# Kernel optimization log

Measured on AMD Instinct MI355X. Metric: run time of the kernel, lower is better.

Reference implementation:

```python
import jax, jax.numpy as jnp
import numpy as np

HEADS = 8
DIM_HEAD = 64
DOWN = 2

def setup_inputs() -> dict:
    key = jax.random.key(0)
    ks = jax.random.split(key, 6)
    shp = (1, 128, 16, 32, 32)
    inner = HEADS * DIM_HEAD  # 512
    return {
        "x": jax.random.normal(ks[0], shp, dtype=jnp.float32),
        "context": jax.random.normal(ks[1], shp, dtype=jnp.float32),
        "Wq": jax.random.normal(ks[2], (inner, 128), dtype=jnp.float32) * 0.02,
        "Wk": jax.random.normal(ks[3], (inner, 128), dtype=jnp.float32) * 0.02,
        "Wv": jax.random.normal(ks[4], (inner, 128), dtype=jnp.float32) * 0.02,
        "Wo": jax.random.normal(ks[5], (128, inner), dtype=jnp.float32) * 0.02,
    }

def _avg_pool3d(c, f):
    b, ch, d, h, w = c.shape
    return c.reshape(b, ch, d // f, f, h // f, f, w // f, f).mean(axis=(3, 5, 7))

def reference(x, context, Wq, Wk, Wv, Wo):
    b, c, d1, h1, w1 = x.shape
    n = d1 * h1 * w1
    scale = DIM_HEAD ** -0.5
    xf = x.reshape(b, c, n)  # [b, c, N]
    # 1x1x1 conv == channel matmul
    q = jnp.einsum('oc,bcn->bon', Wq, xf).reshape(b, HEADS, DIM_HEAD, n)
    q = jnp.swapaxes(q, -2, -1)  # [b, h, N, dh]
    ctx = _avg_pool3d(context, DOWN)
    _, _, d2, h2, w2 = ctx.shape
    m = d2 * h2 * w2
    cf = ctx.reshape(b, c, m)
    k = jnp.einsum('oc,bcm->bom', Wk, cf).reshape(b, HEADS, DIM_HEAD, m)  # [b,h,dh,M]
    v = jnp.einsum('oc,bcm->bom', Wv, cf).reshape(b, HEADS, DIM_HEAD, m)
    v = jnp.swapaxes(v, -2, -1)  # [b, h, M, dh]
    scores = jnp.einsum('bhnd,bhdm->bhnm', q, k) * scale  # [b,h,N,M]
    attn = jax.nn.softmax(scores, axis=-1)
    out = jnp.einsum('bhnm,bhmd->bhnd', attn, v)  # [b,h,N,dh]
    out = jnp.swapaxes(out, -2, -1).reshape(b, HEADS * DIM_HEAD, n)  # [b,inner,N]
    y = jnp.einsum('oc,bcn->bon', Wo, out)
    return y.reshape(b, -1, d1, h1, w1)
```

## Files before the change

kernel.cpp:

```cpp
#include <hip/hip_runtime.h>

#define N_TOK 16384
#define M_TOK 2048
#define NHEADS 8
#define DH 64
#define CIN 128
#define INNER 512

typedef __attribute__((ext_vector_type(8))) short bf16x8;
typedef __attribute__((ext_vector_type(16))) float f32x16;
typedef __attribute__((ext_vector_type(4))) unsigned int u32x4;
typedef __attribute__((ext_vector_type(2))) unsigned int u32x2;

__device__ __forceinline__ unsigned short f2bf(float f) {
    unsigned u = __float_as_uint(f);
    u += 0x7fff + ((u >> 16) & 1);
    return (unsigned short)(u >> 16);
}

__device__ __forceinline__ unsigned cvtpk(float lo, float hi) {
    unsigned r;
    asm("v_cvt_pk_bf16_f32 %0, %1, %2" : "=v"(r) : "v"(lo), "v"(hi));
    return r;
}

__device__ __forceinline__ bf16x8 mk_bf16x8(unsigned a, unsigned b, unsigned c, unsigned d) {
    union { u32x4 w; bf16x8 h; } u;
    u.w = (u32x4){a, b, c, d};
    return u.h;
}

__device__ __forceinline__ void gload16(const void* g, void* l) {
    __builtin_amdgcn_global_load_lds(
        (const __attribute__((address_space(1))) unsigned int*)g,
        (__attribute__((address_space(3))) unsigned int*)l, 16, 0, 0);
}

__global__ __launch_bounds__(256) void prep_k(const float* __restrict__ Wq,
                                              const float* __restrict__ Wo,
                                              const float* __restrict__ cin,
                                              const float* __restrict__ x,
                                              unsigned short* __restrict__ Wqb,
                                              unsigned short* __restrict__ Wob,
                                              float* __restrict__ cout,
                                              unsigned short* __restrict__ xb) {
    __shared__ unsigned short tile[64 * 132];
    const int t = threadIdx.x;
    if (blockIdx.x < 64) {
        int i = (blockIdx.x * 256 + t) * 8;
        const float* src; unsigned short* dst; float sc;
        if (i < 65536) { src = Wq + i; dst = Wqb + i; sc = 0.125f; }
        else           { src = Wo + (i - 65536); dst = Wob + (i - 65536); sc = 1.0f; }
        float4 a = *reinterpret_cast<const float4*>(src);
        float4 b = *reinterpret_cast<const float4*>(src + 4);
        unsigned short u[8] = { f2bf(a.x * sc), f2bf(a.y * sc), f2bf(a.z * sc), f2bf(a.w * sc),
                                f2bf(b.x * sc), f2bf(b.y * sc), f2bf(b.z * sc), f2bf(b.w * sc) };
        *reinterpret_cast<uint4*>(dst) = *reinterpret_cast<uint4*>(u);
    } else if (blockIdx.x < 1088) {
        int idx = (blockIdx.x - 64) * 256 + t;
        int c = idx >> 11, m = idx & 2047;
        int d2 = m >> 8, h2 = (m >> 4) & 15, w2 = m & 15;
        const float* b = cin + c * 16384 + d2 * 2048 + h2 * 64 + w2 * 2;
        float s = b[0] + b[1] + b[32] + b[33] + b[1024] + b[1025] + b[1056] + b[1057];
        cout[idx] = s * 0.125f;
    } else {
        const int xbid = blockIdx.x - 1088;
        const int n0 = (xbid & 127) * 128;
        const int cb = (xbid >> 7) * 64;
#pragma unroll
        for (int cc2 = 0; cc2 < 2; ++cc2)
#pragma unroll
            for (int lp = 0; lp < 4; ++lp) {
                int id = lp * 256 + t;
                int row = id >> 5, ch = id & 31;
                float4 v = *reinterpret_cast<const float4*>(
                    &x[(size_t)(cb + cc2 * 32 + row) * N_TOK + n0 + ch * 4]);
                unsigned short u[4] = { f2bf(v.x), f2bf(v.y), f2bf(v.z), f2bf(v.w) };
                *reinterpret_cast<uint2*>(&tile[(cc2 * 32 + row) * 132 + ch * 4]) =
                    *reinterpret_cast<uint2*>(u);
            }
        __syncthreads();
#pragma unroll
        for (int lp = 0; lp < 4; ++lp) {
            int id = lp * 256 + t;
            int n = id >> 3, cg = id & 7;
            unsigned short u[8];
#pragma unroll
            for (int j = 0; j < 8; ++j) u[j] = tile[(cg * 8 + j) * 132 + n];
            *reinterpret_cast<uint4*>(&xb[(size_t)(n0 + n) * 128 + cb + cg * 8]) =
                *reinterpret_cast<uint4*>(u);
        }
    }
}

__global__ __launch_bounds__(256) void kvproj_k(const float* __restrict__ ctx,
                                                const float* __restrict__ Wk,
                                                const float* __restrict__ Wv,
                                                unsigned short* __restrict__ Kb,
                                                unsigned short* __restrict__ Vb) {
    const int m0 = (blockIdx.x * 256 + threadIdx.x) * 2;
    const int o0 = blockIdx.y * 4;
    const float* W = blockIdx.z ? Wv : Wk;
    float acc[4][2];
#pragma unroll
    for (int j = 0; j < 4; ++j) { acc[j][0] = 0.f; acc[j][1] = 0.f; }
    for (int c4 = 0; c4 < CIN / 4; ++c4) {
        float xa[4][2];
#pragma unroll
        for (int cc = 0; cc < 4; ++cc)
            *reinterpret_cast<float2*>(xa[cc]) =
                *reinterpret_cast<const float2*>(&ctx[(size_t)(c4 * 4 + cc) * M_TOK + m0]);
#pragma unroll
        for (int j = 0; j < 4; ++j) {
            float4 wv = *reinterpret_cast<const float4*>(&W[(o0 + j) * CIN + c4 * 4]);
#pragma unroll
            for (int k = 0; k < 2; ++k) {
                acc[j][k] = fmaf(wv.x, xa[0][k], acc[j][k]);
                acc[j][k] = fmaf(wv.y, xa[1][k], acc[j][k]);
                acc[j][k] = fmaf(wv.z, xa[2][k], acc[j][k]);
                acc[j][k] = fmaf(wv.w, xa[3][k], acc[j][k]);
            }
        }
    }
    if (blockIdx.z) {
#pragma unroll
        for (int j = 0; j < 4; ++j) {
            unsigned w0 = (unsigned)f2bf(acc[j][0]) | ((unsigned)f2bf(acc[j][1]) << 16);
            *reinterpret_cast<unsigned*>(&Vb[(size_t)(o0 + j) * M_TOK + m0]) = w0;
        }
    } else {
        const int h = o0 >> 6, d0 = o0 & 63;
#pragma unroll
        for (int k = 0; k < 2; ++k) {
            unsigned short u[4];
#pragma unroll
            for (int j = 0; j < 4; ++j) u[j] = f2bf(acc[j][k]);
            *reinterpret_cast<uint2*>(&Kb[((size_t)h * M_TOK + m0 + k) * DH + d0]) =
                *reinterpret_cast<uint2*>(u);
        }
    }
}

__global__ __launch_bounds__(256) void qproj_k(const unsigned short* __restrict__ Wqb,
                                               const unsigned short* __restrict__ xb,
                                               unsigned short* __restrict__ Qb) {
    const int t = threadIdx.x;
    const int w = t >> 6, l = t & 63;
    const int la = l & 31, lg = l >> 5;
    const int n = blockIdx.x * 32 + la;

    bf16x8 bx[8];
#pragma unroll
    for (int ks = 0; ks < 8; ++ks)
        bx[ks] = *reinterpret_cast<const bf16x8*>(xb + (size_t)n * 128 + ks * 16 + lg * 8);

    f32x16 acc[4];
#pragma unroll
    for (int os = 0; os < 4; ++os) acc[os] = (f32x16){0,0,0,0,0,0,0,0,0,0,0,0,0,0,0,0};

#pragma unroll
    for (int os = 0; os < 4; ++os) {
        const int row = w * 128 + os * 32 + la;
#pragma unroll
        for (int ks = 0; ks < 8; ++ks) {
            bf16x8 aw = *reinterpret_cast<const bf16x8*>(Wqb + (size_t)row * 128 + ks * 16 + lg * 8);
            acc[os] = __builtin_amdgcn_mfma_f32_32x32x16_bf16(aw, bx[ks], acc[os], 0, 0, 0);
        }
    }
#pragma unroll
    for (int os = 0; os < 4; ++os) {
        const int h = w * 2 + (os >> 1);
        const int dbase = (os & 1) * 32 + 4 * lg;
#pragma unroll
        for (int rr = 0; rr < 4; ++rr) {
            unsigned p0 = cvtpk(acc[os][rr * 4 + 0], acc[os][rr * 4 + 1]);
            unsigned p1 = cvtpk(acc[os][rr * 4 + 2], acc[os][rr * 4 + 3]);
            uint2 pv = make_uint2(p0, p1);
            *reinterpret_cast<uint2*>(&Qb[((size_t)h * N_TOK + n) * DH + dbase + rr * 8]) = pv;
        }
    }
}

__global__ __launch_bounds__(512, 4) void attn_k(const unsigned short* __restrict__ Qb,
                                                 const unsigned short* __restrict__ Kb,
                                                 const unsigned short* __restrict__ Vb,
                                                 unsigned short* __restrict__ Ob) {
    __shared__ __align__(16) char smem[65536];
    __shared__ float rsinv[256];

    const int t = threadIdx.x;
    const int w = t >> 6, l = t & 63;
    const int la = l & 31, lg = l >> 5;
    const int bid = blockIdx.x;
    const int h = bid & 7;
    const int n0 = (bid >> 3) * 256;

    bf16x8 aq[4];
    {
        const unsigned short* qrow = Qb + ((size_t)h * N_TOK + n0 + w * 32 + la) * DH + lg * 8;
#pragma unroll
        for (int ks = 0; ks < 4; ++ks)
            aq[ks] = *reinterpret_cast<const bf16x8*>(qrow + ks * 16);
    }

    const char* gK = (const char*)Kb + (size_t)h * M_TOK * 128;
    const char* gV = (const char*)Vb + (size_t)h * DH * 4096;

    auto stage = [&](int b, int tile) {
        char* buf = smem + b * 32768;
#pragma unroll
        for (int i = 0; i < 2; ++i) {
            int c = t + i * 512;
            int row = c >> 3, o16 = (c & 7) << 4;
            gload16(gK + (size_t)(tile * 128 + row) * 128 + (o16 ^ ((row & 7) << 4)),
                    buf + c * 16);
            int vrow = c >> 4, vo16 = (c & 15) << 4;
            gload16(gV + (size_t)vrow * 4096 + tile * 256 + (vo16 ^ ((vrow & 7) << 4)),
                    buf + 16384 + c * 16);
        }
    };

    f32x16 oacc0 = {0,0,0,0,0,0,0,0,0,0,0,0,0,0,0,0};
    f32x16 oacc1 = {0,0,0,0,0,0,0,0,0,0,0,0,0,0,0,0};
    float rs = 0.f;

    stage(0, 0);
    __syncthreads();

#pragma unroll 2
    for (int mt = 0; mt < M_TOK / 128; ++mt) {
        const int cb = (mt & 1) * 32768;
        if (mt < M_TOK / 128 - 1) stage((mt & 1) ^ 1, mt + 1);

#pragma unroll
        for (int ms = 0; ms < 4; ++ms) {
            f32x16 sacc = {0,0,0,0,0,0,0,0,0,0,0,0,0,0,0,0};
            __builtin_amdgcn_s_setprio(1);
#pragma unroll
            for (int ks = 0; ks < 4; ++ks) {
                const int row = ms * 32 + la;
                bf16x8 ak = *reinterpret_cast<const bf16x8*>(
                    smem + cb + row * 128 + ((32 * ks + 16 * lg) ^ ((row & 7) << 4)));
                sacc = __builtin_amdgcn_mfma_f32_32x32x16_bf16(ak, aq[ks], sacc, 0, 0, 0);
            }
            __builtin_amdgcn_s_setprio(0);
            float p[16];
#pragma unroll
            for (int r = 0; r < 16; ++r) { p[r] = __expf(sacc[r]); rs += p[r]; }
            u32x2 s0 = __builtin_amdgcn_permlane32_swap(cvtpk(p[0], p[1]),  cvtpk(p[4], p[5]),  false, false);
            u32x2 s1 = __builtin_amdgcn_permlane32_swap(cvtpk(p[2], p[3]),  cvtpk(p[6], p[7]),  false, false);
            u32x2 s2 = __builtin_amdgcn_permlane32_swap(cvtpk(p[8], p[9]),  cvtpk(p[12], p[13]), false, false);
            u32x2 s3 = __builtin_amdgcn_permlane32_swap(cvtpk(p[10], p[11]), cvtpk(p[14], p[15]), false, false);
            bf16x8 pa0 = mk_bf16x8(s0.x, s1.x, s0.y, s1.y);
            bf16x8 pa1 = mk_bf16x8(s2.x, s3.x, s2.y, s3.y);
            __builtin_amdgcn_s_setprio(1);
            {
                const int vrow = la, vs = (vrow & 7) << 4;
                const char* vb = smem + cb + 16384 + vrow * 256;
                bf16x8 bv0 = *reinterpret_cast<const bf16x8*>(vb + ((64 * ms + 16 * lg) ^ vs));
                bf16x8 bv1 = *reinterpret_cast<const bf16x8*>(vb + ((64 * ms + 32 + 16 * lg) ^ vs));
                oacc0 = __builtin_amdgcn_mfma_f32_32x32x16_bf16(pa0, bv0, oacc0, 0, 0, 0);
                oacc0 = __builtin_amdgcn_mfma_f32_32x32x16_bf16(pa1, bv1, oacc0, 0, 0, 0);
            }
            {
                const int vrow = 32 + la, vs = (vrow & 7) << 4;
                const char* vb = smem + cb + 16384 + vrow * 256;
                bf16x8 bv0 = *reinterpret_cast<const bf16x8*>(vb + ((64 * ms + 16 * lg) ^ vs));
                bf16x8 bv1 = *reinterpret_cast<const bf16x8*>(vb + ((64 * ms + 32 + 16 * lg) ^ vs));
                oacc1 = __builtin_amdgcn_mfma_f32_32x32x16_bf16(pa0, bv0, oacc1, 0, 0, 0);
                oacc1 = __builtin_amdgcn_mfma_f32_32x32x16_bf16(pa1, bv1, oacc1, 0, 0, 0);
            }
            __builtin_amdgcn_s_setprio(0);
        }
        __syncthreads();
    }

    rs += __shfl_xor(rs, 32);
    if (lg == 0) rsinv[w * 32 + la] = 1.0f / rs;

    float* Ot = reinterpret_cast<float*>(smem);
#pragma unroll
    for (int pass = 0; pass < 2; ++pass) {
        __syncthreads();
        if ((w >> 2) == pass) {
            const int wl = w & 3;
#pragma unroll
            for (int dt = 0; dt < 2; ++dt)
#pragma unroll
                for (int r = 0; r < 16; r += 2) {
                    int d = dt * 32 + la;
                    int n = wl * 32 + (r & 3) + 8 * (r >> 2) + 4 * lg;
                    float2 v;
                    v.x = dt ? oacc1[r] : oacc0[r];
                    v.y = dt ? oacc1[r + 1] : oacc0[r + 1];
                    *reinterpret_cast<float2*>(&Ot[d * 132 + n]) = v;
                }
        }
        __syncthreads();
#pragma unroll
        for (int i = 0; i < 2; ++i) {
            int id = i * 512 + t;
            int n = id & 127, dg = id >> 7;
            float rv = rsinv[pass * 128 + n];
            unsigned q[4];
#pragma unroll
            for (int jj = 0; jj < 4; ++jj) {
                float a = Ot[(dg * 8 + jj * 2) * 132 + n] * rv;
                float b = Ot[(dg * 8 + jj * 2 + 1) * 132 + n] * rv;
                q[jj] = cvtpk(a, b);
            }
            *reinterpret_cast<uint4*>(&Ob[(size_t)(n0 + pass * 128 + n) * INNER + h * 64 + dg * 8]) =
                *reinterpret_cast<uint4*>(q);
        }
    }
}

__global__ __launch_bounds__(256) void yproj_k(const unsigned short* __restrict__ Wob,
                                               const unsigned short* __restrict__ Ob,
                                               float* __restrict__ y) {
    const int t = threadIdx.x;
    const int w = t >> 6, l = t & 63;
    const int la = l & 31, lg = l >> 5;
    const int n = blockIdx.x * 32 + la;
    const int row = w * 32 + la;

    f32x16 acc = {0,0,0,0,0,0,0,0,0,0,0,0,0,0,0,0};
#pragma unroll 8
    for (int ks = 0; ks < 32; ++ks) {
        bf16x8 bo = *reinterpret_cast<const bf16x8*>(Ob + (size_t)n * INNER + ks * 16 + lg * 8);
        bf16x8 aw = *reinterpret_cast<const bf16x8*>(Wob + (size_t)row * INNER + ks * 16 + lg * 8);
        acc = __builtin_amdgcn_mfma_f32_32x32x16_bf16(aw, bo, acc, 0, 0, 0);
    }
#pragma unroll
    for (int rr = 0; rr < 4; ++rr)
#pragma unroll
        for (int q = 0; q < 4; ++q) {
            int o = w * 32 + 4 * lg + rr * 8 + q;
            y[(size_t)o * N_TOK + n] = acc[rr * 4 + q];
        }
}

extern "C" void kernel_launch(void* const* d_in, const int* in_sizes, int n_in,
                              void* d_out, int out_size, void* d_ws, size_t ws_size,
                              hipStream_t stream) {
    const float* x   = (const float*)d_in[0];
    const float* ctx = (const float*)d_in[1];
    const float* Wq  = (const float*)d_in[2];
    const float* Wk  = (const float*)d_in[3];
    const float* Wv  = (const float*)d_in[4];
    const float* Wo  = (const float*)d_in[5];
    float* y = (float*)d_out;

    char* W = (char*)d_ws;
    float* ctxp         = (float*)(W);
    unsigned short* Kb  = (unsigned short*)(W + 1u  * (1 << 20));
    unsigned short* Vb  = (unsigned short*)(W + 3u  * (1 << 20));
    unsigned short* xb  = (unsigned short*)(W + 5u  * (1 << 20));
    unsigned short* Wqb = (unsigned short*)(W + 9u  * (1 << 20));
    unsigned short* Wob = (unsigned short*)(W + 9u  * (1 << 20) + (256 << 10));
    unsigned short* Qb  = (unsigned short*)(W + 10u * (1 << 20));
    unsigned short* Ob  = (unsigned short*)(W + 26u * (1 << 20));

    prep_k<<<dim3(64 + 1024 + 256), 256, 0, stream>>>(Wq, Wo, ctx, x, Wqb, Wob, ctxp, xb);
    kvproj_k<<<dim3(M_TOK / 512, INNER / 4, 2), 256, 0, stream>>>(ctxp, Wk, Wv, Kb, Vb);
    qproj_k<<<dim3(N_TOK / 32), 256, 0, stream>>>(Wqb, xb, Qb);
    attn_k<<<dim3(N_TOK / 256 * NHEADS), 512, 0, stream>>>(Qb, Kb, Vb, Ob);
    yproj_k<<<dim3(N_TOK / 32), 256, 0, stream>>>(Wob, Ob, y);
}
```

Before: 137.0 us.

## Merge K/V and Q projections, use exp2 with folded scale, MFMA row sums

Merges the K/V projection and Q projection kernels into a single launch, splitting work by block index, which removes one kernel launch and lets the two projections run concurrently. The softmax scale is folded with log2(e) into Wq so the attention loop can use the hardware exp2 instruction. Per-row softmax sums are now accumulated with extra MFMAs against a ones vector instead of scalar adds plus a cross-lane shuffle, and normalization moves into the register-to-LDS store. The cost is two additional MFMAs per tile, plus the sums being taken from bf16-rounded probabilities.

```diff
diff --git a/kernel.cpp b/kernel.cpp
--- a/kernel.cpp
+++ b/kernel.cpp
@@ -11,6 +11,14 @@
 typedef __attribute__((ext_vector_type(16))) float f32x16;
 typedef __attribute__((ext_vector_type(4))) unsigned int u32x4;
 typedef __attribute__((ext_vector_type(2))) unsigned int u32x2;
+
+#if __has_builtin(__builtin_amdgcn_exp2f)
+#define QS 0.18033688011112042f
+#define EXPF(x) __builtin_amdgcn_exp2f(x)
+#else
+#define QS 0.125f
+#define EXPF(x) __expf(x)
+#endif
 
 __device__ __forceinline__ unsigned short f2bf(float f) {
     unsigned u = __float_as_uint(f);
@@ -49,7 +57,7 @@
     if (blockIdx.x < 64) {
         int i = (blockIdx.x * 256 + t) * 8;
         const float* src; unsigned short* dst; float sc;
-        if (i < 65536) { src = Wq + i; dst = Wqb + i; sc = 0.125f; }
+        if (i < 65536) { src = Wq + i; dst = Wqb + i; sc = QS; }
         else           { src = Wo + (i - 65536); dst = Wob + (i - 65536); sc = 1.0f; }
         float4 a = *reinterpret_cast<const float4*>(src);
         float4 b = *reinterpret_cast<const float4*>(src + 4);
@@ -93,90 +101,94 @@
     }
 }
 
-__global__ __launch_bounds__(256) void kvproj_k(const float* __restrict__ ctx,
-                                                const float* __restrict__ Wk,
-                                                const float* __restrict__ Wv,
-                                                unsigned short* __restrict__ Kb,
-                                                unsigned short* __restrict__ Vb) {
-    const int m0 = (blockIdx.x * 256 + threadIdx.x) * 2;
-    const int o0 = blockIdx.y * 4;
-    const float* W = blockIdx.z ? Wv : Wk;
-    float acc[4][2];
-#pragma unroll
-    for (int j = 0; j < 4; ++j) { acc[j][0] = 0.f; acc[j][1] = 0.f; }
-    for (int c4 = 0; c4 < CIN / 4; ++c4) {
-        float xa[4][2];
-#pragma unroll
-        for (int cc = 0; cc < 4; ++cc)
-            *reinterpret_cast<float2*>(xa[cc]) =
-                *reinterpret_cast<const float2*>(&ctx[(size_t)(c4 * 4 + cc) * M_TOK + m0]);
-#pragma unroll
-        for (int j = 0; j < 4; ++j) {
-            float4 wv = *reinterpret_cast<const float4*>(&W[(o0 + j) * CIN + c4 * 4]);
+__global__ __launch_bounds__(256) void projs_k(const float* __restrict__ ctx,
+                                               const float* __restrict__ Wk,
+                                               const float* __restrict__ Wv,
+                                               const unsigned short* __restrict__ Wqb,
+                                               const unsigned short* __restrict__ xb,
+                                               unsigned short* __restrict__ Kb,
+                                               unsigned short* __restrict__ Vb,
+                                               unsigned short* __restrict__ Qb) {
+    const int b = blockIdx.x;
+    const int t = threadIdx.x;
+    if (b < 1024) {
+        const int bx = b & 3, by = (b >> 2) & 127, bz = b >> 9;
+        const int m0 = (bx * 256 + t) * 2;
+        const int o0 = by * 4;
+        const float* W = bz ? Wv : Wk;
+        float acc[4][2];
+#pragma unroll
+        for (int j = 0; j < 4; ++j) { acc[j][0] = 0.f; acc[j][1] = 0.f; }
+        for (int c4 = 0; c4 < CIN / 4; ++c4) {
+            float xa[4][2];
+#pragma unroll
+            for (int cc = 0; cc < 4; ++cc)
+                *reinterpret_cast<float2*>(xa[cc]) =
+                    *reinterpret_cast<const float2*>(&ctx[(size_t)(c4 * 4 + cc) * M_TOK + m0]);
+#pragma unroll
+            for (int j = 0; j < 4; ++j) {
+                float4 wv = *reinterpret_cast<const float4*>(&W[(o0 + j) * CIN + c4 * 4]);
+#pragma unroll
+                for (int k = 0; k < 2; ++k) {
+                    acc[j][k] = fmaf(wv.x, xa[0][k], acc[j][k]);
+                    acc[j][k] = fmaf(wv.y, xa[1][k], acc[j][k]);
+                    acc[j][k] = fmaf(wv.z, xa[2][k], acc[j][k]);
+                    acc[j][k] = fmaf(wv.w, xa[3][k], acc[j][k]);
+                }
+            }
+        }
+        if (bz) {
+#pragma unroll
+            for (int j = 0; j < 4; ++j) {
+                unsigned w0 = (unsigned)f2bf(acc[j][0]) | ((unsigned)f2bf(acc[j][1]) << 16);
+                *reinterpret_cast<unsigned*>(&Vb[(size_t)(o0 + j) * M_TOK + m0]) = w0;
+            }
+        } else {
+            const int h = o0 >> 6, d0 = o0 & 63;
 #pragma unroll
             for (int k = 0; k < 2; ++k) {
-                acc[j][k] = fmaf(wv.x, xa[0][k], acc[j][k]);
-                acc[j][k] = fmaf(wv.y, xa[1][k], acc[j][k]);
-                acc[j][k] = fmaf(wv.z, xa[2][k], acc[j][k]);
-                acc[j][k] = fmaf(wv.w, xa[3][k], acc[j][k]);
-            }
-        }
-    }
-    if (blockIdx.z) {
-#pragma unroll
-        for (int j = 0; j < 4; ++j) {
-            unsigned w0 = (unsigned)f2bf(acc[j][0]) | ((unsigned)f2bf(acc[j][1]) << 16);
-            *reinterpret_cast<unsigned*>(&Vb[(size_t)(o0 + j) * M_TOK + m0]) = w0;
+                unsigned short u[4];
+#pragma unroll
+                for (int j = 0; j < 4; ++j) u[j] = f2bf(acc[j][k]);
+                *reinterpret_cast<uint2*>(&Kb[((size_t)h * M_TOK + m0 + k) * DH + d0]) =
+                    *reinterpret_cast<uint2*>(u);
+            }
         }
     } else {
-        const int h = o0 >> 6, d0 = o0 & 63;
-#pragma unroll
-        for (int k = 0; k < 2; ++k) {
-            unsigned short u[4];
-#pragma unroll
-            for (int j = 0; j < 4; ++j) u[j] = f2bf(acc[j][k]);
-            *reinterpret_cast<uint2*>(&Kb[((size_t)h * M_TOK + m0 + k) * DH + d0]) =
-                *reinterpret_cast<uint2*>(u);
-        }
-    }
-}
-
-__global__ __launch_bounds__(256) void qproj_k(const unsigned short* __restrict__ Wqb,
-                                               const unsigned short* __restrict__ xb,
-                                               unsigned short* __restrict__ Qb) {
-    const int t = threadIdx.x;
-    const int w = t >> 6, l = t & 63;
-    const int la = l & 31, lg = l >> 5;
-    const int n = blockIdx.x * 32 + la;
-
-    bf16x8 bx[8];
-#pragma unroll
-    for (int ks = 0; ks < 8; ++ks)
-        bx[ks] = *reinterpret_cast<const bf16x8*>(xb + (size_t)n * 128 + ks * 16 + lg * 8);
-
-    f32x16 acc[4];
-#pragma unroll
-    for (int os = 0; os < 4; ++os) acc[os] = (f32x16){0,0,0,0,0,0,0,0,0,0,0,0,0,0,0,0};
-
-#pragma unroll
-    for (int os = 0; os < 4; ++os) {
-        const int row = w * 128 + os * 32 + la;
-#pragma unroll
-        for (int ks = 0; ks < 8; ++ks) {
-            bf16x8 aw = *reinterpret_cast<const bf16x8*>(Wqb + (size_t)row * 128 + ks * 16 + lg * 8);
-            acc[os] = __builtin_amdgcn_mfma_f32_32x32x16_bf16(aw, bx[ks], acc[os], 0, 0, 0);
-        }
-    }
-#pragma unroll
-    for (int os = 0; os < 4; ++os) {
-        const int h = w * 2 + (os >> 1);
-        const int dbase = (os & 1) * 32 + 4 * lg;
-#pragma unroll
-        for (int rr = 0; rr < 4; ++rr) {
-            unsigned p0 = cvtpk(acc[os][rr * 4 + 0], acc[os][rr * 4 + 1]);
-            unsigned p1 = cvtpk(acc[os][rr * 4 + 2], acc[os][rr * 4 + 3]);
-            uint2 pv = make_uint2(p0, p1);
-            *reinterpret_cast<uint2*>(&Qb[((size_t)h * N_TOK + n) * DH + dbase + rr * 8]) = pv;
+        const int bid = b - 1024;
+        const int w = t >> 6, l = t & 63;
+        const int la = l & 31, lg = l >> 5;
+        const int n = bid * 32 + la;
+
+        bf16x8 bx[8];
+#pragma unroll
+        for (int ks = 0; ks < 8; ++ks)
+            bx[ks] = *reinterpret_cast<const bf16x8*>(xb + (size_t)n * 128 + ks * 16 + lg * 8);
+
+        f32x16 acc[4];
+#pragma unroll
+        for (int os = 0; os < 4; ++os) acc[os] = (f32x16){0,0,0,0,0,0,0,0,0,0,0,0,0,0,0,0};
+
+#pragma unroll
+        for (int os = 0; os < 4; ++os) {
+            const int row = w * 128 + os * 32 + la;
+#pragma unroll
+            for (int ks = 0; ks < 8; ++ks) {
+                bf16x8 aw = *reinterpret_cast<const bf16x8*>(Wqb + (size_t)row * 128 + ks * 16 + lg * 8);
+                acc[os] = __builtin_amdgcn_mfma_f32_32x32x16_bf16(aw, bx[ks], acc[os], 0, 0, 0);
+            }
+        }
+#pragma unroll
+        for (int os = 0; os < 4; ++os) {
+            const int h = w * 2 + (os >> 1);
+            const int dbase = (os & 1) * 32 + 4 * lg;
+#pragma unroll
+            for (int rr = 0; rr < 4; ++rr) {
+                unsigned p0 = cvtpk(acc[os][rr * 4 + 0], acc[os][rr * 4 + 1]);
+                unsigned p1 = cvtpk(acc[os][rr * 4 + 2], acc[os][rr * 4 + 3]);
+                uint2 pv = make_uint2(p0, p1);
+                *reinterpret_cast<uint2*>(&Qb[((size_t)h * N_TOK + n) * DH + dbase + rr * 8]) = pv;
+            }
         }
     }
 }
@@ -186,7 +198,6 @@
                                                  const unsigned short* __restrict__ Vb,
                                                  unsigned short* __restrict__ Ob) {
     __shared__ __align__(16) char smem[65536];
-    __shared__ float rsinv[256];
 
     const int t = threadIdx.x;
     const int w = t >> 6, l = t & 63;
@@ -202,6 +213,8 @@
         for (int ks = 0; ks < 4; ++ks)
             aq[ks] = *reinterpret_cast<const bf16x8*>(qrow + ks * 16);
     }
+
+    const bf16x8 vone = mk_bf16x8(0x3F803F80u, 0x3F803F80u, 0x3F803F80u, 0x3F803F80u);
 
     const char* gK = (const char*)Kb + (size_t)h * M_TOK * 128;
     const char* gV = (const char*)Vb + (size_t)h * DH * 4096;
@@ -222,7 +235,7 @@
 
     f32x16 oacc0 = {0,0,0,0,0,0,0,0,0,0,0,0,0,0,0,0};
     f32x16 oacc1 = {0,0,0,0,0,0,0,0,0,0,0,0,0,0,0,0};
-    float rs = 0.f;
+    f32x16 oaccS = {0,0,0,0,0,0,0,0,0,0,0,0,0,0,0,0};
 
     stage(0, 0);
     __syncthreads();
@@ -246,7 +259,7 @@
             __builtin_amdgcn_s_setprio(0);
             float p[16];
 #pragma unroll
-            for (int r = 0; r < 16; ++r) { p[r] = __expf(sacc[r]); rs += p[r]; }
+            for (int r = 0; r < 16; ++r) p[r] = EXPF(sacc[r]);
             u32x2 s0 = __builtin_amdgcn_permlane32_swap(cvtpk(p[0], p[1]),  cvtpk(p[4], p[5]),  false, false);
             u32x2 s1 = __builtin_amdgcn_permlane32_swap(cvtpk(p[2], p[3]),  cvtpk(p[6], p[7]),  false, false);
             u32x2 s2 = __builtin_amdgcn_permlane32_swap(cvtpk(p[8], p[9]),  cvtpk(p[12], p[13]), false, false);
@@ -254,6 +267,8 @@
             bf16x8 pa0 = mk_bf16x8(s0.x, s1.x, s0.y, s1.y);
             bf16x8 pa1 = mk_bf16x8(s2.x, s3.x, s2.y, s3.y);
             __builtin_amdgcn_s_setprio(1);
+            oaccS = __builtin_amdgcn_mfma_f32_32x32x16_bf16(pa0, vone, oaccS, 0, 0, 0);
+            oaccS = __builtin_amdgcn_mfma_f32_32x32x16_bf16(pa1, vone, oaccS, 0, 0, 0);
             {
                 const int vrow = la, vs = (vrow & 7) << 4;
                 const char* vb = smem + cb + 16384 + vrow * 256;
@@ -275,8 +290,9 @@
         __syncthreads();
     }
 
-    rs += __shfl_xor(rs, 32);
-    if (lg == 0) rsinv[w * 32 + la] = 1.0f / rs;
+    float inv[16];
+#pragma unroll
+    for (int r = 0; r < 16; ++r) inv[r] = __builtin_amdgcn_rcpf(oaccS[r]);
 
     float* Ot = reinterpret_cast<float*>(smem);
 #pragma unroll
@@ -291,8 +307,8 @@
                     int d = dt * 32 + la;
                     int n = wl * 32 + (r & 3) + 8 * (r >> 2) + 4 * lg;
                     float2 v;
-                    v.x = dt ? oacc1[r] : oacc0[r];
-                    v.y = dt ? oacc1[r + 1] : oacc0[r + 1];
+                    v.x = (dt ? oacc1[r] : oacc0[r]) * inv[r];
+                    v.y = (dt ? oacc1[r + 1] : oacc0[r + 1]) * inv[r + 1];
                     *reinterpret_cast<float2*>(&Ot[d * 132 + n]) = v;
                 }
         }
@@ -301,14 +317,11 @@
         for (int i = 0; i < 2; ++i) {
             int id = i * 512 + t;
             int n = id & 127, dg = id >> 7;
-            float rv = rsinv[pass * 128 + n];
             unsigned q[4];
 #pragma unroll
-            for (int jj = 0; jj < 4; ++jj) {
-                float a = Ot[(dg * 8 + jj * 2) * 132 + n] * rv;
-                float b = Ot[(dg * 8 + jj * 2 + 1) * 132 + n] * rv;
-                q[jj] = cvtpk(a, b);
-            }
+            for (int jj = 0; jj < 4; ++jj)
+                q[jj] = cvtpk(Ot[(dg * 8 + jj * 2) * 132 + n],
+                              Ot[(dg * 8 + jj * 2 + 1) * 132 + n]);
             *reinterpret_cast<uint4*>(&Ob[(size_t)(n0 + pass * 128 + n) * INNER + h * 64 + dg * 8]) =
                 *reinterpret_cast<uint4*>(q);
         }
@@ -362,8 +375,7 @@
     unsigned short* Ob  = (unsigned short*)(W + 26u * (1 << 20));
 
     prep_k<<<dim3(64 + 1024 + 256), 256, 0, stream>>>(Wq, Wo, ctx, x, Wqb, Wob, ctxp, xb);
-    kvproj_k<<<dim3(M_TOK / 512, INNER / 4, 2), 256, 0, stream>>>(ctxp, Wk, Wv, Kb, Vb);
-    qproj_k<<<dim3(N_TOK / 32), 256, 0, stream>>>(Wqb, xb, Qb);
+    projs_k<<<dim3(1024 + N_TOK / 32), 256, 0, stream>>>(ctxp, Wk, Wv, Wqb, xb, Kb, Vb, Qb);
     attn_k<<<dim3(N_TOK / 256 * NHEADS), 512, 0, stream>>>(Qb, Kb, Vb, Ob);
     yproj_k<<<dim3(N_TOK / 32), 256, 0, stream>>>(Wob, Ob, y);
 }
```

Result: faster. 130.7 us (-4.6%).
